# Kernel tuning notes

Measured on AMD Instinct MI355X. Metric: run time of the kernel, lower is better.

Reference implementation:

```python
import jax, jax.numpy as jnp
import numpy as np

B, S, D, H = 4, 2048, 1024, 16
HS = D // H          # head size 64
DF = 4 * D           # ffn hidden 4096
EPS = 1e-5


def _layer_norm(x, g, b):
    mu = jnp.mean(x, axis=-1, keepdims=True)
    var = jnp.var(x, axis=-1, keepdims=True)
    return (x - mu) * jax.lax.rsqrt(var + EPS) * g + b


def setup_inputs() -> dict:
    key = jax.random.key(0)
    ks = jax.random.split(key, 12)
    s_d = 1.0 / np.sqrt(D)
    s_f = 1.0 / np.sqrt(DF)
    return {
        "x": jax.random.normal(ks[0], (B, S, D), jnp.float32),
        # per-head q/k/v projections, batched over heads: [H, D, HS]
        "wq": jax.random.uniform(ks[1], (H, D, HS), jnp.float32, -s_d, s_d),
        "wk": jax.random.uniform(ks[2], (H, D, HS), jnp.float32, -s_d, s_d),
        "wv": jax.random.uniform(ks[3], (H, D, HS), jnp.float32, -s_d, s_d),
        "proj_w": jax.random.uniform(ks[4], (D, D), jnp.float32, -s_d, s_d),
        "proj_b": jax.random.uniform(ks[5], (D,), jnp.float32, -s_d, s_d),
        "ff1_w": jax.random.uniform(ks[6], (D, DF), jnp.float32, -s_d, s_d),
        "ff1_b": jax.random.uniform(ks[7], (DF,), jnp.float32, -s_d, s_d),
        "ff2_w": jax.random.uniform(ks[8], (DF, D), jnp.float32, -s_f, s_f),
        "ff2_b": jax.random.uniform(ks[9], (D,), jnp.float32, -s_f, s_f),
        "ln1_g": jnp.ones((D,), jnp.float32),
        "ln1_b": jnp.zeros((D,), jnp.float32),
        "ln2_g": jnp.ones((D,), jnp.float32),
        "ln2_b": jnp.zeros((D,), jnp.float32),
    }


def reference(x, wq, wk, wv, proj_w, proj_b, ff1_w, ff1_b, ff2_w, ff2_b,
              ln1_g, ln1_b, ln2_g, ln2_b):
    # --- multi-head causal self-attention on ln1(x), all heads batched ---
    h = _layer_norm(x, ln1_g, ln1_b)                      # [B,S,D]
    q = jnp.einsum("bsd,hde->bhse", h, wq)                # [B,H,S,HS]
    k = jnp.einsum("bsd,hde->bhse", h, wk)
    v = jnp.einsum("bsd,hde->bhse", h, wv)
    scale = HS ** -0.5
    scores = jnp.einsum("bhse,bhte->bhst", q, k) * scale  # [B,H,S,S]
    causal = jnp.tril(jnp.ones((S, S), bool))
    scores = jnp.where(causal, scores, jnp.finfo(scores.dtype).min)
    att = jax.nn.softmax(scores, axis=-1)
    o = jnp.einsum("bhst,bhte->bhse", att, v)             # [B,H,S,HS]
    o = o.transpose(0, 2, 1, 3).reshape(B, S, D)          # concat heads
    sa = o @ proj_w + proj_b
    x = x + sa
    # --- FFN on ln2(x) ---
    h2 = _layer_norm(x, ln2_g, ln2_b)
    ff = jax.nn.relu(h2 @ ff1_w + ff1_b) @ ff2_w + ff2_b
    return x + ff
```

## Files before the change

kernel.cpp:

```cpp
#include <hip/hip_runtime.h>
#include <hip/hip_bf16.h>

#define BB 4
#define SS 2048
#define DD 1024
#define HH 16
#define HSZ 64
#define DFF 4096

typedef short short8 __attribute__((ext_vector_type(8)));
typedef float f32x4 __attribute__((ext_vector_type(4)));
typedef unsigned short us4 __attribute__((ext_vector_type(4)));

#define AS1 __attribute__((address_space(1)))
#define AS3 __attribute__((address_space(3)))

__device__ __forceinline__ unsigned short f2bf(float f) {
    return __bfloat16_as_ushort(__float2bfloat16(f));
}

__global__ __launch_bounds__(256) void pack_qkv_kernel(
    const float* __restrict__ wq, const float* __restrict__ wk,
    const float* __restrict__ wv, __hip_bfloat16* __restrict__ out)
{
    __shared__ float tile[64][65];
    const int bid = blockIdx.x;
    const int kt = bid & 15, hh = (bid >> 4) & 15, sel = bid >> 8;
    const float* src = (sel == 0) ? wq : (sel == 1) ? wk : wv;
    src += (size_t)hh * (DD * HSZ) + (size_t)kt * 64 * HSZ;
    const int tx = threadIdx.x & 63, ty = threadIdx.x >> 6;
    #pragma unroll
    for (int r = 0; r < 64; r += 4)
        tile[r + ty][tx] = src[(size_t)(r + ty) * HSZ + tx];
    __syncthreads();
    unsigned short* o = (unsigned short*)out + (size_t)(sel * DD + hh * 64) * DD + kt * 64;
    #pragma unroll
    for (int r = 0; r < 64; r += 4) {
        int e = r + ty;
        o[(size_t)e * DD + tx] = f2bf(tile[tx][e]);
    }
}

__global__ __launch_bounds__(256) void pack_T_kernel(
    const float* __restrict__ in, __hip_bfloat16* __restrict__ out, int K, int N)
{
    __shared__ float tile[64][65];
    const int nb = N >> 6;
    const int tn0 = (blockIdx.x % nb) << 6, tk0 = (blockIdx.x / nb) << 6;
    const int tx = threadIdx.x & 63, ty = threadIdx.x >> 6;
    #pragma unroll
    for (int r = 0; r < 64; r += 4)
        tile[r + ty][tx] = in[(size_t)(tk0 + r + ty) * N + tn0 + tx];
    __syncthreads();
    unsigned short* o = (unsigned short*)out;
    #pragma unroll
    for (int r = 0; r < 64; r += 4) {
        int n = r + ty;
        o[(size_t)(tn0 + n) * K + tk0 + tx] = f2bf(tile[tx][n]);
    }
}

__global__ __launch_bounds__(256) void ln_kernel(
    const float* __restrict__ x, const float* __restrict__ g,
    const float* __restrict__ b, __hip_bfloat16* __restrict__ out)
{
    int row = blockIdx.x;
    int t = threadIdx.x;
    const float4* xr = (const float4*)(x + (size_t)row * DD);
    float4 v = xr[t];
    float s = v.x + v.y + v.z + v.w;
    float ss = v.x * v.x + v.y * v.y + v.z * v.z + v.w * v.w;
    #pragma unroll
    for (int off = 32; off; off >>= 1) {
        s += __shfl_xor(s, off, 64);
        ss += __shfl_xor(ss, off, 64);
    }
    __shared__ float red[8];
    int w = t >> 6, lane = t & 63;
    if (lane == 0) { red[w] = s; red[4 + w] = ss; }
    __syncthreads();
    s = red[0] + red[1] + red[2] + red[3];
    ss = red[4] + red[5] + red[6] + red[7];
    float mu = s * (1.f / DD);
    float var = ss * (1.f / DD) - mu * mu;
    float rs = rsqrtf(var + 1e-5f);
    float4 gv = ((const float4*)g)[t];
    float4 bv = ((const float4*)b)[t];
    ushort4 pk = make_ushort4(
        f2bf((v.x - mu) * rs * gv.x + bv.x),
        f2bf((v.y - mu) * rs * gv.y + bv.y),
        f2bf((v.z - mu) * rs * gv.z + bv.z),
        f2bf((v.w - mu) * rs * gv.w + bv.w));
    *(ushort4*)((unsigned short*)out + (size_t)row * DD + t * 4) = pk;
}

template<int BN, bool BIAS, bool RELU, bool RES, bool OUTF32>
__global__ __launch_bounds__(512) void gemm_kernel(
    const __hip_bfloat16* __restrict__ A, const __hip_bfloat16* __restrict__ BT,
    const float* __restrict__ bias, const float* __restrict__ res,
    void* __restrict__ Cout, int M, int N, int K, int nbx)
{
    constexpr int NB = BN / 128;
    constexpr int NREP = BN / 64;
    __shared__ uint4 Ah[2][2][1024];
    __shared__ uint4 Bh[2][NB][1024];

    const int tid = threadIdx.x;
    const int lane = tid & 63;
    const int w = tid >> 6;
    const int lr = lane & 15, g = lane >> 4;
    const int nwg = gridDim.x;
    const int cpx = nwg >> 3;
    const int wg = blockIdx.x;
    const int swz = (wg & 7) * cpx + (wg >> 3);
    const int bx = swz % nbx, by = swz / nbx;
    const int row0 = by * 256, col0 = bx * BN;
    const int wm = w >> 2, wn = w & 3;
    const int NT = K >> 6;

    f32x4 acc0[4][NREP] = {};
    f32x4 acc1[4][NREP] = {};
    short8 bfr[NREP][2];

    auto stageA = [&](int buf, int half, int t) {
        const int k0 = t * 64;
        #pragma unroll
        for (int j = 0; j < 2; ++j) {
            int s = j * 512 + tid;
            int r = s >> 3;
            int c = (s & 7) ^ (r & 7);
            const __hip_bfloat16* src = A + (size_t)(row0 + half * 128 + r) * K + k0 + c * 8;
            __builtin_amdgcn_global_load_lds((const AS1 void*)src,
                (AS3 void*)(&Ah[buf][half][j * 512 + (tid & ~63)]), 16, 0, 0);
        }
    };
    auto stageB = [&](int buf, int half, int t) {
        const int k0 = t * 64;
        #pragma unroll
        for (int j = 0; j < 2; ++j) {
            int s = j * 512 + tid;
            int r = s >> 3;
            int c = (s & 7) ^ (r & 7);
            const __hip_bfloat16* src = BT + (size_t)(col0 + half * 128 + r) * K + k0 + c * 8;
            __builtin_amdgcn_global_load_lds((const AS1 void*)src,
                (AS3 void*)(&Bh[buf][half][j * 512 + (tid & ~63)]), 16, 0, 0);
        }
    };
    auto loadB = [&](int buf) {
        const int hb = (NB == 2) ? (wn >> 1) : 0;
        const int cb = (NB == 2) ? ((wn & 1) * 64) : (wn * 32);
        #pragma unroll
        for (int n = 0; n < NREP; ++n) {
            int c = cb + n * 16 + lr;
            #pragma unroll
            for (int kk = 0; kk < 2; ++kk)
                bfr[n][kk] = *(const short8*)&Bh[buf][hb][c * 8 + ((kk * 4 + g) ^ (c & 7))];
        }
    };
    auto phase = [&](auto& acc, int buf, int mh) {
        short8 af[4][2];
        #pragma unroll
        for (int mi = 0; mi < 4; ++mi) {
            int r = wm * 64 + mi * 16 + lr;
            #pragma unroll
            for (int kk = 0; kk < 2; ++kk)
                af[mi][kk] = *(const short8*)&Ah[buf][mh][r * 8 + ((kk * 4 + g) ^ (r & 7))];
        }
        asm volatile("s_waitcnt lgkmcnt(0)" ::: "memory");
        __builtin_amdgcn_sched_barrier(0);
        __builtin_amdgcn_s_setprio(1);
        #pragma unroll
        for (int mi = 0; mi < 4; ++mi)
            #pragma unroll
            for (int n = 0; n < NREP; ++n)
                #pragma unroll
                for (int kk = 0; kk < 2; ++kk)
                    acc[mi][n] = __builtin_amdgcn_mfma_f32_16x16x32_bf16(
                        af[mi][kk], bfr[n][kk], acc[mi][n], 0, 0, 0);
        __builtin_amdgcn_s_setprio(0);
    };

    stageA(0, 0, 0);
    stageB(0, 0, 0);
    if constexpr (NB == 2) stageB(0, 1, 0);
    stageA(0, 1, 0);
    stageA(1, 0, 1);
    if constexpr (NB == 2) stageB(1, 0, 1);

    for (int t = 0; t < NT; ++t) {
        const int buf = t & 1;
        if (t < NT - 1) {
            if constexpr (NB == 2) asm volatile("s_waitcnt vmcnt(4)" ::: "memory");
            else                   asm volatile("s_waitcnt vmcnt(2)" ::: "memory");
        } else {
            asm volatile("s_waitcnt vmcnt(0)" ::: "memory");
        }
        __builtin_amdgcn_s_barrier();
        __builtin_amdgcn_sched_barrier(0);
        if (t + 1 < NT) {
            if constexpr (NB == 2) { stageB(buf ^ 1, 1, t + 1); stageA(buf ^ 1, 1, t + 1); }
            else                   { stageB(buf ^ 1, 0, t + 1); stageA(buf ^ 1, 1, t + 1); }
        }
        loadB(buf);
        phase(acc0, buf, 0);
        if (t < NT - 1) {
            if constexpr (NB == 2) asm volatile("s_waitcnt vmcnt(8)" ::: "memory");
            else                   asm volatile("s_waitcnt vmcnt(6)" ::: "memory");
        } else {
            asm volatile("s_waitcnt vmcnt(0)" ::: "memory");
        }
        __builtin_amdgcn_s_barrier();
        __builtin_amdgcn_sched_barrier(0);
        if (t + 2 < NT) {
            stageA(buf, 0, t + 2);
            if constexpr (NB == 2) stageB(buf, 0, t + 2);
        }
        phase(acc1, buf, 1);
    }

    auto store = [&](auto& acc, int mh) {
        #pragma unroll
        for (int mi = 0; mi < 4; ++mi) {
            #pragma unroll
            for (int j = 0; j < 4; ++j) {
                int rr = row0 + mh * 128 + wm * 64 + mi * 16 + g * 4 + j;
                #pragma unroll
                for (int n = 0; n < NREP; ++n) {
                    int cc = col0 + wn * (NREP * 16) + n * 16 + lr;
                    float vv = acc[mi][n][j];
                    if (BIAS) vv += bias[cc];
                    if (RELU) vv = fmaxf(vv, 0.f);
                    if (RES) vv += res[(size_t)rr * N + cc];
                    if (OUTF32) ((float*)Cout)[(size_t)rr * N + cc] = vv;
                    else ((__hip_bfloat16*)Cout)[(size_t)rr * N + cc] = __float2bfloat16(vv);
                }
            }
        }
    };
    store(acc0, 0);
    store(acc1, 1);
}

__device__ __forceinline__ void stage_K(
    const unsigned short* __restrict__ qkvu, size_t rowbase, int h, int kv0, int tl,
    unsigned short* __restrict__ Kb)
{
    int kv = tl >> 2, c = tl & 3;
    const unsigned short* src = qkvu + rowbase + (size_t)(kv0 + kv) * 3072 + DD + h * HSZ + c * 16;
    uint4 v0 = *(const uint4*)src;
    uint4 v1 = *(const uint4*)(src + 8);
    int sw = kv & 7;
    *(uint4*)&Kb[kv * 64 + ((2 * c) ^ sw) * 8] = v0;
    *(uint4*)&Kb[kv * 64 + ((2 * c + 1) ^ sw) * 8] = v1;
}

__device__ __forceinline__ void stage_V(
    const unsigned short* __restrict__ qkvu, size_t rowbase, int h, int kv0, int tl,
    unsigned short* __restrict__ Vb)
{
    int bkv = ((tl >> 6) << 2) | (tl & 3);
    int bd = (tl >> 2) & 15;
    const unsigned short* src = qkvu + rowbase + (size_t)(kv0 + bkv * 4) * 3072 + 2 * DD + h * HSZ + bd * 4;
    us4 r0 = *(const us4*)src;
    us4 r1 = *(const us4*)(src + 3072);
    us4 r2 = *(const us4*)(src + 2 * 3072);
    us4 r3 = *(const us4*)(src + 3 * 3072);
    #pragma unroll
    for (int cc = 0; cc < 4; ++cc) {
        int d = bd * 4 + cc;
        us4 wv = { r0[cc], r1[cc], r2[cc], r3[cc] };
        *(us4*)&Vb[d * 64 + (((bkv >> 1) ^ (d & 7)) * 8) + (bkv & 1) * 4] = wv;
    }
}

__device__ __forceinline__ void flash_tile(
    const unsigned short* __restrict__ Kb, const unsigned short* __restrict__ Vb,
    unsigned short* __restrict__ Pw, const short8* qfc, int qgc, int kv0, int q, int g,
    float& m_run, float& l_run, f32x4* oacc, bool masked)
{
    f32x4 st[4] = {};
    __builtin_amdgcn_s_setprio(1);
    #pragma unroll
    for (int tt = 0; tt < 4; ++tt) {
        #pragma unroll
        for (int kk = 0; kk < 2; ++kk) {
            short8 kf = *(const short8*)&Kb[(tt * 16 + q) * 64 + ((4 * kk + g) ^ (q & 7)) * 8];
            st[tt] = __builtin_amdgcn_mfma_f32_16x16x32_bf16(kf, qfc[kk], st[tt], 0, 0, 0);
        }
    }
    __builtin_amdgcn_s_setprio(0);

    const float SC = 0.1803368801111731f;
    float mt = -1e30f;
    if (masked) {
        #pragma unroll
        for (int tt = 0; tt < 4; ++tt)
            #pragma unroll
            for (int j = 0; j < 4; ++j) {
                float s = st[tt][j] * SC;
                int kvg = kv0 + tt * 16 + g * 4 + j;
                s = (kvg <= qgc) ? s : -1e30f;
                st[tt][j] = s;
                mt = fmaxf(mt, s);
            }
    } else {
        #pragma unroll
        for (int tt = 0; tt < 4; ++tt)
            #pragma unroll
            for (int j = 0; j < 4; ++j) {
                float s = st[tt][j] * SC;
                st[tt][j] = s;
                mt = fmaxf(mt, s);
            }
    }
    mt = fmaxf(mt, __shfl_xor(mt, 16, 64));
    mt = fmaxf(mt, __shfl_xor(mt, 32, 64));

    bool defer = __all(mt <= m_run + 11.0f);
    if (!defer) {
        float m_new = fmaxf(m_run, mt);
        float corr = exp2f(m_run - m_new);
        #pragma unroll
        for (int j = 0; j < 4; ++j) {
            float cj = __shfl(corr, g * 4 + j, 64);
            #pragma unroll
            for (int dn = 0; dn < 4; ++dn)
                oacc[dn][j] *= cj;
        }
        l_run *= corr;
        m_run = m_new;
    }

    float lsum = 0.f;
    #pragma unroll
    for (int tt = 0; tt < 4; ++tt)
        #pragma unroll
        for (int j = 0; j < 4; ++j) {
            float p = exp2f(st[tt][j] - m_run);
            st[tt][j] = p;
            lsum += p;
        }
    lsum += __shfl_xor(lsum, 16, 64);
    lsum += __shfl_xor(lsum, 32, 64);
    l_run += lsum;

    __builtin_amdgcn_s_setprio(1);
    #pragma unroll
    for (int kk = 0; kk < 2; ++kk) {
        #pragma unroll
        for (int rt = 0; rt < 2; ++rt) {
            int tt = kk * 2 + rt;
            unsigned int lo = ((unsigned int)f2bf(st[tt][1]) << 16) | (unsigned int)f2bf(st[tt][0]);
            unsigned int hi = ((unsigned int)f2bf(st[tt][3]) << 16) | (unsigned int)f2bf(st[tt][2]);
            uint2 pk = make_uint2(lo, hi);
            *(uint2*)&Pw[q * 32 + ((2 * rt + (g >> 1)) ^ ((q >> 1) & 3)) * 8 + (g & 1) * 4] = pk;
        }
        short8 pf = *(const short8*)&Pw[q * 32 + (g ^ ((q >> 1) & 3)) * 8];
        #pragma unroll
        for (int dn = 0; dn < 4; ++dn) {
            short8 vf = *(const short8*)&Vb[(dn * 16 + q) * 64 + ((4 * kk + g) ^ (q & 7)) * 8];
            oacc[dn] = __builtin_amdgcn_mfma_f32_16x16x32_bf16(pf, vf, oacc[dn], 0, 0, 0);
        }
    }
    __builtin_amdgcn_s_setprio(0);
}

__global__ __launch_bounds__(512, 4) void attn_kernel(
    const __hip_bfloat16* __restrict__ qkv, __hip_bfloat16* __restrict__ o)
{
    __shared__ unsigned short K_lds[2][64 * 64];
    __shared__ unsigned short Vt_lds[2][64 * 64];
    __shared__ unsigned short P_lds[8 * 512];

    const int t = threadIdx.x;
    const int lane = t & 63, w = t >> 6;
    const int grp = w >> 2, wq4 = w & 3, tl = t & 255;
    const int q = lane & 15, g = lane >> 4;
    const int wg = blockIdx.x;
    const int swzb = (wg & 7) * 128 + (wg >> 3);
    const int pq = swzb & 15;
    const int h = (swzb >> 4) & 15;
    const int b = swzb >> 8;
    const int qtA = pq, qtB = 31 - pq;
    const int qt1 = grp ? qtB : qtA;
    const unsigned short* qkvu = (const unsigned short*)qkv;
    const size_t rowbase = (size_t)(b * SS) * 3072;
    unsigned short* Kb = K_lds[grp];
    unsigned short* Vb = Vt_lds[grp];
    unsigned short* Pw = &P_lds[w * 512];
    unsigned short* op = (unsigned short*)o;

    int qt_cur = qt1;
    int qgc = qt_cur * 64 + wq4 * 16 + q;
    short8 qfc[2];
    #pragma unroll
    for (int kk = 0; kk < 2; ++kk)
        qfc[kk] = *(const short8*)(qkvu + rowbase + (size_t)qgc * 3072 + h * HSZ + kk * 32 + g * 8);

    f32x4 oacc[4] = {};
    float m_run = -1e30f, l_run = 0.f;

    for (int it = 0; it <= pq; ++it) {
        __syncthreads();
        if (grp == 0) stage_K(qkvu, rowbase, h, it * 64, tl, K_lds[0]);
        else          stage_V(qkvu, rowbase, h, it * 64, tl, Vt_lds[0]);
        __syncthreads();
        flash_tile(K_lds[0], Vt_lds[0], Pw, qfc, qgc, it * 64, q, g, m_run, l_run, oacc,
                   it == qt_cur);
    }

    if (grp == 0) {
        #pragma unroll
        for (int j = 0; j < 4; ++j) {
            float lj = __shfl(l_run, g * 4 + j, 64);
            float inv = 1.f / lj;
            int orow = qtA * 64 + wq4 * 16 + g * 4 + j;
            #pragma unroll
            for (int dn = 0; dn < 4; ++dn)
                op[(size_t)(b * SS + orow) * DD + h * HSZ + dn * 16 + q] = f2bf(oacc[dn][j] * inv);
        }
        qt_cur = qtB;
        qgc = qtB * 64 + wq4 * 16 + q;
        #pragma unroll
        for (int kk = 0; kk < 2; ++kk)
            qfc[kk] = *(const short8*)(qkvu + rowbase + (size_t)qgc * 3072 + h * HSZ + kk * 32 + g * 8);
        m_run = -1e30f; l_run = 0.f;
        #pragma unroll
        for (int dn = 0; dn < 4; ++dn) oacc[dn] = f32x4{0.f, 0.f, 0.f, 0.f};
    }

    for (int it2 = 0; it2 < 16 - pq; ++it2) {
        int tile = grp ? (pq + 1 + it2) : (16 + it2);
        bool active = grp ? (tile <= 15) : true;
        __syncthreads();
        if (active) {
            stage_K(qkvu, rowbase, h, tile * 64, tl, Kb);
            stage_V(qkvu, rowbase, h, tile * 64, tl, Vb);
        }
        __syncthreads();
        if (active) flash_tile(Kb, Vb, Pw, qfc, qgc, tile * 64, q, g, m_run, l_run, oacc,
                               tile == qt_cur);
    }

    __syncthreads();
    float* obuf = (float*)K_lds;
    float* mlbuf = (float*)P_lds;
    if (grp == 0) {
        #pragma unroll
        for (int dn = 0; dn < 4; ++dn)
            #pragma unroll
            for (int j = 0; j < 4; ++j)
                obuf[wq4 * 1024 + lane * 16 + dn * 4 + j] = oacc[dn][j];
        if (g == 0) { mlbuf[wq4 * 32 + q] = m_run; mlbuf[wq4 * 32 + 16 + q] = l_run; }
    }
    __syncthreads();
    if (grp == 1) {
        float mA = mlbuf[wq4 * 32 + q];
        float lA = mlbuf[wq4 * 32 + 16 + q];
        float mM = fmaxf(m_run, mA);
        float sB = exp2f(m_run - mM);
        float sA = exp2f(mA - mM);
        float lM = l_run * sB + lA * sA;
        #pragma unroll
        for (int j = 0; j < 4; ++j) {
            float sBj = __shfl(sB, g * 4 + j, 64);
            float sAj = __shfl(sA, g * 4 + j, 64);
            float lMj = __shfl(lM, g * 4 + j, 64);
            float inv = 1.f / lMj;
            int orow = qtB * 64 + wq4 * 16 + g * 4 + j;
            #pragma unroll
            for (int dn = 0; dn < 4; ++dn) {
                float oA = obuf[wq4 * 1024 + lane * 16 + dn * 4 + j];
                float vv = (oacc[dn][j] * sBj + oA * sAj) * inv;
                op[(size_t)(b * SS + orow) * DD + h * HSZ + dn * 16 + q] = f2bf(vv);
            }
        }
    }
}

extern "C" void kernel_launch(void* const* d_in, const int* in_sizes, int n_in,
                              void* d_out, int out_size, void* d_ws, size_t ws_size,
                              hipStream_t stream)
{
    const float* x      = (const float*)d_in[0];
    const float* wq     = (const float*)d_in[1];
    const float* wk     = (const float*)d_in[2];
    const float* wv     = (const float*)d_in[3];
    const float* proj_w = (const float*)d_in[4];
    const float* proj_b = (const float*)d_in[5];
    const float* ff1_w  = (const float*)d_in[6];
    const float* ff1_b  = (const float*)d_in[7];
    const float* ff2_w  = (const float*)d_in[8];
    const float* ff2_b  = (const float*)d_in[9];
    const float* ln1_g  = (const float*)d_in[10];
    const float* ln1_b  = (const float*)d_in[11];
    const float* ln2_g  = (const float*)d_in[12];
    const float* ln2_b  = (const float*)d_in[13];
    float* out = (float*)d_out;

    char* ws = (char*)d_ws;
    const size_t MB = 1ull << 20;
    __hip_bfloat16* h     = (__hip_bfloat16*)(ws);
    __hip_bfloat16* qkv   = (__hip_bfloat16*)(ws + 16 * MB);
    __hip_bfloat16* obuf  = (__hip_bfloat16*)(ws + 64 * MB);
    float*          x1    = (float*)(ws + 80 * MB);
    __hip_bfloat16* wqkvT = (__hip_bfloat16*)(ws + 112 * MB);
    __hip_bfloat16* projT = (__hip_bfloat16*)(ws + 118 * MB);
    __hip_bfloat16* ff1T  = (__hip_bfloat16*)(ws + 120 * MB);
    __hip_bfloat16* ff2T  = (__hip_bfloat16*)(ws + 128 * MB);
    __hip_bfloat16* f1    = (__hip_bfloat16*)(ws + 16 * MB);

    const int ROWS = BB * SS;

    pack_qkv_kernel<<<768, 256, 0, stream>>>(wq, wk, wv, wqkvT);
    pack_T_kernel<<<(DD / 64) * (DD / 64), 256, 0, stream>>>(proj_w, projT, DD, DD);
    pack_T_kernel<<<(DFF / 64) * (DD / 64), 256, 0, stream>>>(ff1_w, ff1T, DD, DFF);
    pack_T_kernel<<<(DD / 64) * (DFF / 64), 256, 0, stream>>>(ff2_w, ff2T, DFF, DD);

    ln_kernel<<<ROWS, 256, 0, stream>>>(x, ln1_g, ln1_b, h);
    gemm_kernel<128, false, false, false, false><<<(ROWS / 256) * (3 * DD / 128), 512, 0, stream>>>(
        h, wqkvT, nullptr, nullptr, qkv, ROWS, 3 * DD, DD, 3 * DD / 128);
    attn_kernel<<<BB * HH * 16, 512, 0, stream>>>(qkv, obuf);
    gemm_kernel<128, true, false, true, true><<<(ROWS / 256) * (DD / 128), 512, 0, stream>>>(
        obuf, projT, proj_b, x, x1, ROWS, DD, DD, DD / 128);
    ln_kernel<<<ROWS, 256, 0, stream>>>(x1, ln2_g, ln2_b, h);
    gemm_kernel<256, true, true, false, false><<<(ROWS / 256) * (DFF / 256), 512, 0, stream>>>(
        h, ff1T, ff1_b, nullptr, f1, ROWS, DFF, DD, DFF / 256);
    gemm_kernel<128, true, false, true, true><<<(ROWS / 256) * (DD / 128), 512, 0, stream>>>(
        f1, ff2T, ff2_b, x1, out, ROWS, DD, DFF, DD / 128);
}
```

Measured before the change: 415.7 us.

## Merge weight packing, store residual in bf16, async K staging in attention

```diff
diff --git a/kernel.cpp b/kernel.cpp
--- a/kernel.cpp
+++ b/kernel.cpp
@@ -18,41 +18,47 @@
 __device__ __forceinline__ unsigned short f2bf(float f) {
     return __bfloat16_as_ushort(__float2bfloat16(f));
 }
-
-__global__ __launch_bounds__(256) void pack_qkv_kernel(
+__device__ __forceinline__ float bf2f(unsigned short u) {
+    return __uint_as_float(((unsigned int)u) << 16);
+}
+
+__global__ __launch_bounds__(256) void pack_all_kernel(
     const float* __restrict__ wq, const float* __restrict__ wk,
-    const float* __restrict__ wv, __hip_bfloat16* __restrict__ out)
+    const float* __restrict__ wv, const float* __restrict__ proj_w,
+    const float* __restrict__ ff1_w, const float* __restrict__ ff2_w,
+    __hip_bfloat16* __restrict__ wqkvT, __hip_bfloat16* __restrict__ projT,
+    __hip_bfloat16* __restrict__ ff1T, __hip_bfloat16* __restrict__ ff2T)
 {
     __shared__ float tile[64][65];
     const int bid = blockIdx.x;
-    const int kt = bid & 15, hh = (bid >> 4) & 15, sel = bid >> 8;
-    const float* src = (sel == 0) ? wq : (sel == 1) ? wk : wv;
-    src += (size_t)hh * (DD * HSZ) + (size_t)kt * 64 * HSZ;
     const int tx = threadIdx.x & 63, ty = threadIdx.x >> 6;
-    #pragma unroll
-    for (int r = 0; r < 64; r += 4)
-        tile[r + ty][tx] = src[(size_t)(r + ty) * HSZ + tx];
-    __syncthreads();
-    unsigned short* o = (unsigned short*)out + (size_t)(sel * DD + hh * 64) * DD + kt * 64;
-    #pragma unroll
-    for (int r = 0; r < 64; r += 4) {
-        int e = r + ty;
-        o[(size_t)e * DD + tx] = f2bf(tile[tx][e]);
-    }
-}
-
-__global__ __launch_bounds__(256) void pack_T_kernel(
-    const float* __restrict__ in, __hip_bfloat16* __restrict__ out, int K, int N)
-{
-    __shared__ float tile[64][65];
+
+    if (bid < 768) {
+        const int kt = bid & 15, hh = (bid >> 4) & 15, sel = bid >> 8;
+        const float* src = (sel == 0) ? wq : (sel == 1) ? wk : wv;
+        src += (size_t)hh * (DD * HSZ) + (size_t)kt * 64 * HSZ;
+        #pragma unroll
+        for (int r = 0; r < 64; r += 4)
+            tile[r + ty][tx] = src[(size_t)(r + ty) * HSZ + tx];
+        __syncthreads();
+        unsigned short* o = (unsigned short*)wqkvT + (size_t)(sel * DD + hh * 64) * DD + kt * 64;
+        #pragma unroll
+        for (int r = 0; r < 64; r += 4) {
+            int e = r + ty;
+            o[(size_t)e * DD + tx] = f2bf(tile[tx][e]);
+        }
+        return;
+    }
+    const float* in; unsigned short* o; int K, N, idx;
+    if (bid < 1024)      { in = proj_w; o = (unsigned short*)projT; K = DD;  N = DD;  idx = bid - 768; }
+    else if (bid < 2048) { in = ff1_w;  o = (unsigned short*)ff1T;  K = DD;  N = DFF; idx = bid - 1024; }
+    else                 { in = ff2_w;  o = (unsigned short*)ff2T;  K = DFF; N = DD;  idx = bid - 2048; }
     const int nb = N >> 6;
-    const int tn0 = (blockIdx.x % nb) << 6, tk0 = (blockIdx.x / nb) << 6;
-    const int tx = threadIdx.x & 63, ty = threadIdx.x >> 6;
+    const int tn0 = (idx % nb) << 6, tk0 = (idx / nb) << 6;
     #pragma unroll
     for (int r = 0; r < 64; r += 4)
         tile[r + ty][tx] = in[(size_t)(tk0 + r + ty) * N + tn0 + tx];
     __syncthreads();
-    unsigned short* o = (unsigned short*)out;
     #pragma unroll
     for (int r = 0; r < 64; r += 4) {
         int n = r + ty;
@@ -60,14 +66,20 @@
     }
 }
 
+template<bool INBF16>
 __global__ __launch_bounds__(256) void ln_kernel(
-    const float* __restrict__ x, const float* __restrict__ g,
+    const void* __restrict__ xin, const float* __restrict__ g,
     const float* __restrict__ b, __hip_bfloat16* __restrict__ out)
 {
     int row = blockIdx.x;
     int t = threadIdx.x;
-    const float4* xr = (const float4*)(x + (size_t)row * DD);
-    float4 v = xr[t];
+    float4 v;
+    if (INBF16) {
+        ushort4 u = ((const ushort4*)((const unsigned short*)xin + (size_t)row * DD))[t];
+        v = make_float4(bf2f(u.x), bf2f(u.y), bf2f(u.z), bf2f(u.w));
+    } else {
+        v = ((const float4*)((const float*)xin + (size_t)row * DD))[t];
+    }
     float s = v.x + v.y + v.z + v.w;
     float ss = v.x * v.x + v.y * v.y + v.z * v.z + v.w * v.w;
     #pragma unroll
@@ -94,10 +106,10 @@
     *(ushort4*)((unsigned short*)out + (size_t)row * DD + t * 4) = pk;
 }
 
-template<int BN, bool BIAS, bool RELU, bool RES, bool OUTF32>
+template<int BN, bool BIAS, bool RELU, bool RES, bool OUTF32, bool RESBF16>
 __global__ __launch_bounds__(512) void gemm_kernel(
     const __hip_bfloat16* __restrict__ A, const __hip_bfloat16* __restrict__ BT,
-    const float* __restrict__ bias, const float* __restrict__ res,
+    const float* __restrict__ bias, const void* __restrict__ res,
     void* __restrict__ Cout, int M, int N, int K, int nbx)
 {
     constexpr int NB = BN / 128;
@@ -230,7 +242,10 @@
                     float vv = acc[mi][n][j];
                     if (BIAS) vv += bias[cc];
                     if (RELU) vv = fmaxf(vv, 0.f);
-                    if (RES) vv += res[(size_t)rr * N + cc];
+                    if (RES) {
+                        if (RESBF16) vv += bf2f(((const unsigned short*)res)[(size_t)rr * N + cc]);
+                        else         vv += ((const float*)res)[(size_t)rr * N + cc];
+                    }
                     if (OUTF32) ((float*)Cout)[(size_t)rr * N + cc] = vv;
                     else ((__hip_bfloat16*)Cout)[(size_t)rr * N + cc] = __float2bfloat16(vv);
                 }
@@ -241,17 +256,19 @@
     store(acc1, 1);
 }
 
-__device__ __forceinline__ void stage_K(
+__device__ __forceinline__ void stage_K_async(
     const unsigned short* __restrict__ qkvu, size_t rowbase, int h, int kv0, int tl,
     unsigned short* __restrict__ Kb)
 {
-    int kv = tl >> 2, c = tl & 3;
-    const unsigned short* src = qkvu + rowbase + (size_t)(kv0 + kv) * 3072 + DD + h * HSZ + c * 16;
-    uint4 v0 = *(const uint4*)src;
-    uint4 v1 = *(const uint4*)(src + 8);
-    int sw = kv & 7;
-    *(uint4*)&Kb[kv * 64 + ((2 * c) ^ sw) * 8] = v0;
-    *(uint4*)&Kb[kv * 64 + ((2 * c + 1) ^ sw) * 8] = v1;
+    #pragma unroll
+    for (int j = 0; j < 2; ++j) {
+        int p = j * 256 + tl;
+        int kv = p >> 3, ch = p & 7;
+        const unsigned short* src = qkvu + rowbase + (size_t)(kv0 + kv) * 3072 + DD
+                                    + h * HSZ + ((ch ^ (kv & 7)) * 8);
+        __builtin_amdgcn_global_load_lds((const AS1 void*)src,
+            (AS3 void*)(Kb + ((size_t)(j * 256 + (tl & ~63)) << 3)), 16, 0, 0);
+    }
 }
 
 __device__ __forceinline__ void stage_V(
@@ -402,7 +419,7 @@
 
     for (int it = 0; it <= pq; ++it) {
         __syncthreads();
-        if (grp == 0) stage_K(qkvu, rowbase, h, it * 64, tl, K_lds[0]);
+        if (grp == 0) stage_K_async(qkvu, rowbase, h, it * 64, tl, K_lds[0]);
         else          stage_V(qkvu, rowbase, h, it * 64, tl, Vt_lds[0]);
         __syncthreads();
         flash_tile(K_lds[0], Vt_lds[0], Pw, qfc, qgc, it * 64, q, g, m_run, l_run, oacc,
@@ -434,7 +451,7 @@
         bool active = grp ? (tile <= 15) : true;
         __syncthreads();
         if (active) {
-            stage_K(qkvu, rowbase, h, tile * 64, tl, Kb);
+            stage_K_async(qkvu, rowbase, h, tile * 64, tl, Kb);
             stage_V(qkvu, rowbase, h, tile * 64, tl, Vb);
         }
         __syncthreads();
@@ -503,7 +520,7 @@
     __hip_bfloat16* h     = (__hip_bfloat16*)(ws);
     __hip_bfloat16* qkv   = (__hip_bfloat16*)(ws + 16 * MB);
     __hip_bfloat16* obuf  = (__hip_bfloat16*)(ws + 64 * MB);
-    float*          x1    = (float*)(ws + 80 * MB);
+    __hip_bfloat16* x1b   = (__hip_bfloat16*)(ws + 80 * MB);
     __hip_bfloat16* wqkvT = (__hip_bfloat16*)(ws + 112 * MB);
     __hip_bfloat16* projT = (__hip_bfloat16*)(ws + 118 * MB);
     __hip_bfloat16* ff1T  = (__hip_bfloat16*)(ws + 120 * MB);
@@ -512,20 +529,18 @@
 
     const int ROWS = BB * SS;
 
-    pack_qkv_kernel<<<768, 256, 0, stream>>>(wq, wk, wv, wqkvT);
-    pack_T_kernel<<<(DD / 64) * (DD / 64), 256, 0, stream>>>(proj_w, projT, DD, DD);
-    pack_T_kernel<<<(DFF / 64) * (DD / 64), 256, 0, stream>>>(ff1_w, ff1T, DD, DFF);
-    pack_T_kernel<<<(DD / 64) * (DFF / 64), 256, 0, stream>>>(ff2_w, ff2T, DFF, DD);
-
-    ln_kernel<<<ROWS, 256, 0, stream>>>(x, ln1_g, ln1_b, h);
-    gemm_kernel<128, false, false, false, false><<<(ROWS / 256) * (3 * DD / 128), 512, 0, stream>>>(
+    pack_all_kernel<<<3072, 256, 0, stream>>>(wq, wk, wv, proj_w, ff1_w, ff2_w,
+                                              wqkvT, projT, ff1T, ff2T);
+
+    ln_kernel<false><<<ROWS, 256, 0, stream>>>(x, ln1_g, ln1_b, h);
+    gemm_kernel<128, false, false, false, false, false><<<(ROWS / 256) * (3 * DD / 128), 512, 0, stream>>>(
         h, wqkvT, nullptr, nullptr, qkv, ROWS, 3 * DD, DD, 3 * DD / 128);
     attn_kernel<<<BB * HH * 16, 512, 0, stream>>>(qkv, obuf);
-    gemm_kernel<128, true, false, true, true><<<(ROWS / 256) * (DD / 128), 512, 0, stream>>>(
-        obuf, projT, proj_b, x, x1, ROWS, DD, DD, DD / 128);
-    ln_kernel<<<ROWS, 256, 0, stream>>>(x1, ln2_g, ln2_b, h);
-    gemm_kernel<256, true, true, false, false><<<(ROWS / 256) * (DFF / 256), 512, 0, stream>>>(
+    gemm_kernel<128, true, false, true, false, false><<<(ROWS / 256) * (DD / 128), 512, 0, stream>>>(
+        obuf, projT, proj_b, x, x1b, ROWS, DD, DD, DD / 128);
+    ln_kernel<true><<<ROWS, 256, 0, stream>>>(x1b, ln2_g, ln2_b, h);
+    gemm_kernel<256, true, true, false, false, false><<<(ROWS / 256) * (DFF / 256), 512, 0, stream>>>(
         h, ff1T, ff1_b, nullptr, f1, ROWS, DFF, DD, DFF / 256);
-    gemm_kernel<128, true, false, true, true><<<(ROWS / 256) * (DD / 128), 512, 0, stream>>>(
-        f1, ff2T, ff2_b, x1, out, ROWS, DD, DFF, DD / 128);
-}
+    gemm_kernel<128, true, false, true, true, true><<<(ROWS / 256) * (DD / 128), 512, 0, stream>>>(
+        f1, ff2T, ff2_b, x1b, out, ROWS, DD, DFF, DD / 128);
+}
```

After: 416.0 us. No clear change (+0.1%).
